# Optimization experiments

Measured on AMD Instinct MI355X. Metric: run time of the kernel, lower is better.

Reference implementation:

```python
import jax, jax.numpy as jnp
import numpy as np

B, T, C, U = 64, 250, 1024, 512


def setup_inputs() -> dict:
    key = jax.random.key(0)
    ks = jax.random.split(key, 9)
    inputs = jax.random.normal(ks[0], (B, T, C), dtype=jnp.float32)
    # contiguous padding mask: True for valid positions
    seq_len = jax.random.randint(ks[1], (B,), T // 2, T + 1)
    mask = jnp.arange(T)[None, :] < seq_len[:, None]
    s_in = 1.0 / np.sqrt(C)
    s_rec = 1.0 / np.sqrt(U)
    Wf = jax.random.normal(ks[2], (C, 3 * U), dtype=jnp.float32) * s_in
    Uf = jax.random.normal(ks[3], (U, 3 * U), dtype=jnp.float32) * s_rec
    bf = jnp.zeros((2, 3 * U), dtype=jnp.float32)  # [input_bias, recurrent_bias] (reset_after=True)
    Wb = jax.random.normal(ks[4], (C, 3 * U), dtype=jnp.float32) * s_in
    Ub = jax.random.normal(ks[5], (U, 3 * U), dtype=jnp.float32) * s_rec
    bb = jnp.zeros((2, 3 * U), dtype=jnp.float32)
    return {"inputs": inputs, "mask": mask, "Wf": Wf, "Uf": Uf, "bf": bf,
            "Wb": Wb, "Ub": Ub, "bb": bb}


def _gru(x_tbc, m_tb, W, Uk, b):
    """Keras GRU v2 (reset_after=True) with masking. x_tbc: [T,B,C], m_tb: [T,B]."""
    # precompute input projections for all timesteps: [T,B,3U]
    xg = jnp.einsum('tbc,cg->tbg', x_tbc, W) + b[0]

    def step(h, inp):
        xg_t, m_t = inp
        hg = h @ Uk + b[1]  # [B,3U]
        xz, xr, xh = jnp.split(xg_t, 3, axis=-1)
        hz, hr, hh = jnp.split(hg, 3, axis=-1)
        z = jax.nn.sigmoid(xz + hz)
        r = jax.nn.sigmoid(xr + hr)
        c = jnp.tanh(xh + r * hh)
        h_new = z * h + (1.0 - z) * c
        h_new = jnp.where(m_t[:, None], h_new, h)  # carry state through masked steps
        return h_new, h_new

    h0 = jnp.zeros((x_tbc.shape[1], Uk.shape[0]), x_tbc.dtype)
    hT, ys = jax.lax.scan(step, h0, (xg, m_tb))
    return ys, hT  # ys: [T,B,U], hT: [B,U]


def reference(inputs, mask, Wf, Uf, bf, Wb, Ub, bb):
    x_t = jnp.transpose(inputs, (1, 0, 2))  # [T,B,C]
    m_t = mask.T  # [T,B]
    y_f, h_f = _gru(x_t, m_t, Wf, Uf, bf)
    # go_backwards: process reversed sequence, then reverse outputs back
    y_b, h_b = _gru(x_t[::-1], m_t[::-1], Wb, Ub, bb)
    y_b = y_b[::-1]
    seq_out = jnp.transpose(jnp.concatenate([y_f, y_b], axis=-1), (1, 0, 2))  # [B,T,2U]
    state_out = jnp.concatenate([h_f, h_b], axis=-1)  # [B,2U]
    return seq_out, state_out
```

## Files before the change

### kernel.cpp

```cpp
#include <hip/hip_runtime.h>
#include <cmath>

#define BB 64
#define TT 250
#define CC 1024
#define GG 1536

typedef unsigned long long u64t;
typedef unsigned int uint32;
typedef unsigned short ushort16;
typedef __attribute__((ext_vector_type(8))) short short8v;
typedef __attribute__((ext_vector_type(4))) float f32x4;

#define O_XGF 0
#define O_XGB 24576000
#define O_UT  49152000
#define O_MF  50724864
#define O_VH  50740864
#define O_WT  51003008
#define O_HINT 54148736

__device__ __forceinline__ unsigned short f2bf(float f) {
  unsigned u = __float_as_uint(f);
  return (unsigned short)((u + 0x7fffu + ((u >> 16) & 1u)) >> 16);
}
__device__ __forceinline__ float bf2f(unsigned short h) {
  return __uint_as_float((unsigned)h << 16);
}
__device__ __forceinline__ void cvt2(float a, float b, uint32& hi, uint32& lo) {
  unsigned short ha = f2bf(a), hb = f2bf(b);
  hi = (uint32)ha | ((uint32)hb << 16);
  lo = (uint32)f2bf(a - bf2f(ha)) | ((uint32)f2bf(b - bf2f(hb)) << 16);
}

__global__ __launch_bounds__(256) void wt_build(
    const float* __restrict__ Wf, const float* __restrict__ Wb,
    ushort16* __restrict__ wt_hi, ushort16* __restrict__ wt_lo)
{
  __shared__ float tile[64][65];
  const int k0 = blockIdx.x * 64;
  const int n0 = blockIdx.y * 64;
  const int d  = blockIdx.z;
  const float* W = d ? Wb : Wf;
  const int l = threadIdx.x & 63, w = threadIdx.x >> 6;
  #pragma unroll
  for (int j = 0; j < 16; j++) {
    int r = j*4 + w;
    tile[r][l] = W[(size_t)(k0+r)*GG + n0 + l];
  }
  __syncthreads();
  #pragma unroll
  for (int j = 0; j < 16; j++) {
    int r = j*4 + w;
    float f = tile[l][r];
    unsigned short h = f2bf(f);
    size_t o = (size_t)(d*GG + n0 + r)*1024 + k0 + l;
    wt_hi[o] = h;
    wt_lo[o] = f2bf(f - bf2f(h));
  }
}

#define LDFRAG(dst, arr, row, kg) do { \
    union { uint4 u; short8v s; } r_; \
    r_.u = *(const uint4*)&arr[(row)*40 + ((kg) << 3)]; \
    dst = r_.s; } while (0)

__global__ __launch_bounds__(256) void fused_prologue(
    const float* __restrict__ X,
    const ushort16* __restrict__ wt_hi, const ushort16* __restrict__ wt_lo,
    const float* __restrict__ bf, const float* __restrict__ bb,
    float* __restrict__ xgf, float* __restrict__ xgb,
    const unsigned char* __restrict__ mraw,
    float* __restrict__ mf, u64t* __restrict__ vh, uint32* __restrict__ hints,
    const float* __restrict__ Uf, const float* __restrict__ Ub,
    float* __restrict__ ut)
{
  __shared__ __align__(16) char sm[40960];
  const int tid = threadIdx.x;
  const int bidx = blockIdx.x;

  if (bidx >= 3512) {
    float (*tile)[65] = (float(*)[65])sm;
    const int q  = bidx - 3512;
    const int k0 = (q & 7) * 64;
    const int n0 = ((q >> 3) % 24) * 64;
    const int d  = q / 192;
    const float* Um = d ? Ub : Uf;
    const int l = tid & 63, w = tid >> 6;
    #pragma unroll
    for (int j = 0; j < 16; j++) {
      int r = j*4 + w;
      tile[r][l] = Um[(size_t)(k0+r)*GG + n0 + l];
    }
    __syncthreads();
    #pragma unroll
    for (int j = 0; j < 16; j++) {
      int r = j*4 + w;
      int n = n0 + r, u = n & 511, g = n >> 9;
      ut[(size_t)(((d << 9) | u)*3 + g)*512 + k0 + l] = tile[l][r];
    }
    return;
  }
  if (bidx >= 3000) {
    int idx = (bidx - 3000) * 256 + tid;
    if (idx < 131072)
      __hip_atomic_store(&vh[idx], 0ULL, __ATOMIC_RELAXED, __HIP_MEMORY_SCOPE_AGENT);
    if (idx < 1024)
      __hip_atomic_store(&hints[idx], 0u, __ATOMIC_RELAXED, __HIP_MEMORY_SCOPE_AGENT);
    if (idx < BB*TT) {
      int b = idx / TT, t = idx - b*TT;
      bool bytefmt = (mraw[1] == 1);
      bool mv = bytefmt ? (mraw[idx] != 0) : (((const int*)mraw)[idx] != 0);
      mf[t*BB + b] = mv ? 1.0f : 0.0f;
    }
    return;
  }

  ushort16* Ah = (ushort16*)sm;
  ushort16* Al = Ah + 128*40;
  ushort16* Bh = Al + 128*40;
  ushort16* Bl = Bh + 128*40;
  const int l  = tid & 63;
  const int wv = tid >> 6;
  const int wm = wv & 1;
  const int wn = wv >> 1;
  const int t0 = (bidx / 24) * 2;
  const int n0 = (bidx % 24) * 128;
  const int d  = (n0 >= GG) ? 1 : 0;
  const int nl0 = n0 - d*GG;
  const float* bias = d ? bb : bf;
  float* xg = d ? xgb : xgf;

  const int sr = tid >> 1;
  const int sk = (tid & 1) << 4;
  const ushort16* whp = wt_hi + (size_t)(d*GG + nl0 + sr)*1024 + sk;
  const ushort16* wlp = wt_lo + (size_t)(d*GG + nl0 + sr)*1024 + sk;
  const int mrow = (sr & 63)*TT + t0 + (sr >> 6);
  const float* xp = X + (size_t)mrow*CC + sk;

  f32x4 acc[4][4];
  #pragma unroll
  for (int i = 0; i < 4; i++)
    #pragma unroll
    for (int j = 0; j < 4; j++) acc[i][j] = (f32x4){0.f,0.f,0.f,0.f};

  const int kg = l >> 4;
  for (int k0 = 0; k0 < CC; k0 += 32) {
    uint4 ha = *(const uint4*)(whp + k0);
    uint4 hb = *(const uint4*)(whp + k0 + 8);
    uint4 la = *(const uint4*)(wlp + k0);
    uint4 lb = *(const uint4*)(wlp + k0 + 8);
    float4 x0 = *(const float4*)(xp + k0);
    float4 x1 = *(const float4*)(xp + k0 + 4);
    float4 x2 = *(const float4*)(xp + k0 + 8);
    float4 x3 = *(const float4*)(xp + k0 + 12);
    __syncthreads();
    {
      *(uint4*)&Ah[sr*40 + sk]     = ha;
      *(uint4*)&Ah[sr*40 + sk + 8] = hb;
      *(uint4*)&Al[sr*40 + sk]     = la;
      *(uint4*)&Al[sr*40 + sk + 8] = lb;
      uint32 bhv[8], blv[8];
      cvt2(x0.x, x0.y, bhv[0], blv[0]); cvt2(x0.z, x0.w, bhv[1], blv[1]);
      cvt2(x1.x, x1.y, bhv[2], blv[2]); cvt2(x1.z, x1.w, bhv[3], blv[3]);
      cvt2(x2.x, x2.y, bhv[4], blv[4]); cvt2(x2.z, x2.w, bhv[5], blv[5]);
      cvt2(x3.x, x3.y, bhv[6], blv[6]); cvt2(x3.z, x3.w, bhv[7], blv[7]);
      *(uint4*)&Bh[sr*40 + sk]     = make_uint4(bhv[0], bhv[1], bhv[2], bhv[3]);
      *(uint4*)&Bh[sr*40 + sk + 8] = make_uint4(bhv[4], bhv[5], bhv[6], bhv[7]);
      *(uint4*)&Bl[sr*40 + sk]     = make_uint4(blv[0], blv[1], blv[2], blv[3]);
      *(uint4*)&Bl[sr*40 + sk + 8] = make_uint4(blv[4], blv[5], blv[6], blv[7]);
    }
    __syncthreads();
    short8v afh[4], afl[4], bfh[4], bfl[4];
    #pragma unroll
    for (int i = 0; i < 4; i++) {
      const int rA = wn*64 + i*16 + (l & 15);
      LDFRAG(afh[i], Ah, rA, kg);
      LDFRAG(afl[i], Al, rA, kg);
      const int rB = wm*64 + i*16 + (l & 15);
      LDFRAG(bfh[i], Bh, rB, kg);
      LDFRAG(bfl[i], Bl, rB, kg);
    }
    #pragma unroll
    for (int i = 0; i < 4; i++)
      #pragma unroll
      for (int j = 0; j < 4; j++) {
        acc[i][j] = __builtin_amdgcn_mfma_f32_16x16x32_bf16(afh[i], bfh[j], acc[i][j], 0, 0, 0);
        acc[i][j] = __builtin_amdgcn_mfma_f32_16x16x32_bf16(afh[i], bfl[j], acc[i][j], 0, 0, 0);
        acc[i][j] = __builtin_amdgcn_mfma_f32_16x16x32_bf16(afl[i], bfh[j], acc[i][j], 0, 0, 0);
      }
  }
  const int t = t0 + wm;
  #pragma unroll
  for (int i = 0; i < 4; i++) {
    const int ugl = wn*64 + i*16 + ((l >> 4) << 2);
    #pragma unroll
    for (int r = 0; r < 4; r++) {
      const int n = nl0 + ugl + r;
      const float bv = bias[n];
      float* orow = xg + (size_t)t*98304 + ((size_t)(n >> 9) << 15) + ((n & 511) << 6);
      #pragma unroll
      for (int j = 0; j < 4; j++)
        orow[j*16 + (l & 15)] = acc[i][j][r] + bv;
    }
  }
}

__global__ __launch_bounds__(512, 2) void gru_scan(
    float* xgf, float* xgb,
    const float* __restrict__ ut, const float* __restrict__ bf,
    const float* __restrict__ bb, const float* __restrict__ mf,
    u64t* vh, uint32* hints, float* __restrict__ out)
{
  __shared__ __align__(16) unsigned short Bhi[2][8192];
  __shared__ __align__(16) unsigned short Blo[2][8192];
  const int tid = threadIdx.x;
  const int l   = tid & 63;
  const int wv  = tid >> 6;
  const int bid = blockIdx.x;
  const int d     = bid >> 6;
  const int mb    = (bid >> 2) & 15;
  const int btile = bid & 3;

  short8v af_hi[16], af_lo[16];
  {
    const int row = (wv << 4) | (l & 15);
    const int g   = row & 3;
    const int ua  = (mb << 5) | (row >> 2);
    const int kg_ = (l >> 4) << 3;
    if (g < 3) {
      const float* ap = ut + (((size_t)(((d << 9) | ua) * 3 + g)) << 9);
      #pragma unroll
      for (int ks = 0; ks < 16; ks++)
        #pragma unroll
        for (int j = 0; j < 8; j++) {
          float f = ap[(ks << 5) + kg_ + j];
          unsigned short h = f2bf(f);
          af_hi[ks][j] = (short)h;
          af_lo[ks][j] = (short)f2bf(f - bf2f(h));
        }
    } else {
      #pragma unroll
      for (int ks = 0; ks < 16; ks++)
        #pragma unroll
        for (int j = 0; j < 8; j++) { af_hi[ks][j] = 0; af_lo[ks][j] = 0; }
    }
  }

  const int u  = (mb << 5) | (wv << 2) | (l >> 4);
  const int b  = (btile << 4) | (l & 15);
  const float* bias = (d ? bb : bf) + GG;
  const float b1z = bias[u], b1r = bias[512+u], b1h = bias[1024+u];
  float* xg = d ? xgb : xgf;
  float hprev = 0.0f;

  const int kc  = tid >> 4;
  const int blw = tid & 15;
  const int cb  = (btile << 4) | blw;
  const int ksub_w = kc >> 1;
  const int qbase  = (kc & 1) << 1;
  const int boff = ((l & 15) << 6) + (((l >> 4) ^ ((l >> 1) & 3)) << 4);

  const u64t* hg = (const u64t*)(hints + (((d << 2) | btile) << 7));
  uint32* myhint = hints + ((((d << 2) | btile) << 7) | (mb << 3) | wv);

  float xzA, xrA, xhA, mA, xzB, xrB, xhB, mB;
  {
    const int tA = d ? (TT-1) : 0;
    const float* p = xg + (size_t)tA*98304 + (u << 6) + b;
    xzA = p[0]; xrA = p[32768]; xhA = p[65536]; mA = mf[tA*BB + b];
    const int tB = d ? (TT-2) : 1;
    const float* q = xg + (size_t)tB*98304 + (u << 6) + b;
    xzB = q[0]; xrB = q[32768]; xhB = q[65536]; mB = mf[tB*BB + b];
  }

  for (int s = 0; s < TT; s++) {
    const unsigned us_ = (unsigned)s;
    const int t = d ? (TT-1-s) : s;
    u64t* vin = vh + (size_t)((((unsigned)s & 1u) << 1) | (unsigned)d) * 32768;

    u64t v[16];
    #pragma unroll
    for (int i = 0; i < 16; i++)
      v[i] = __hip_atomic_load(vin + ((kc << 4) + i)*64 + cb, __ATOMIC_RELAXED, __HIP_MEMORY_SCOPE_AGENT);
    int bad = 0;
    #pragma unroll
    for (int i = 0; i < 16; i++) bad |= ((unsigned)(v[i] >> 32) < us_) ? 1 : 0;
    if (__any(bad)) {
      while (true) {
        u64t hv = __hip_atomic_load(&hg[l], __ATOMIC_RELAXED, __HIP_MEMORY_SCOPE_AGENT);
        if (__all(((unsigned)hv >= us_) && ((unsigned)(hv >> 32) >= us_))) break;
        __builtin_amdgcn_s_sleep(1);
      }
      asm volatile("" ::: "memory");
      while (true) {
        #pragma unroll
        for (int i = 0; i < 16; i++)
          if ((unsigned)(v[i] >> 32) < us_)
            v[i] = __hip_atomic_load(vin + ((kc << 4) + i)*64 + cb, __ATOMIC_RELAXED, __HIP_MEMORY_SCOPE_AGENT);
        int bad2 = 0;
        #pragma unroll
        for (int i = 0; i < 16; i++) bad2 |= ((unsigned)(v[i] >> 32) < us_) ? 1 : 0;
        if (!__any(bad2)) break;
        __builtin_amdgcn_s_sleep(1);
      }
    }

    unsigned short* BhiS = Bhi[s & 1];
    unsigned short* BloS = Blo[s & 1];
    #pragma unroll
    for (int half = 0; half < 2; half++) {
      uint32 hw[4], lw[4];
      #pragma unroll
      for (int p = 0; p < 4; p++) {
        u64t v0 = v[(half << 3) + (p << 1)];
        u64t v1 = v[(half << 3) + (p << 1) + 1];
        hw[p] = (uint32)((v0 >> 16) & 0xffffu) | ((uint32)((v1 >> 16) & 0xffffu) << 16);
        lw[p] = (uint32)(v0 & 0xffffu)         | ((uint32)(v1 & 0xffffu) << 16);
      }
      const int phys = (qbase + half) ^ ((blw >> 1) & 3);
      const int off = (ksub_w << 10) + (blw << 6) + (phys << 4);
      *(uint4*)((char*)BhiS + off) = make_uint4(hw[0], hw[1], hw[2], hw[3]);
      *(uint4*)((char*)BloS + off) = make_uint4(lw[0], lw[1], lw[2], lw[3]);
    }
    __syncthreads();

    float xzC = 0.f, xrC = 0.f, xhC = 0.f, mC = 0.f;
    if (s+2 < TT) {
      const int t2 = d ? (TT-3-s) : (s+2);
      const float* xp = xg + (size_t)t2*98304 + (u << 6) + b;
      xzC = xp[0]; xrC = xp[32768]; xhC = xp[65536];
      mC  = mf[t2*BB + b];
    }

    f32x4 acc0 = {0.f,0.f,0.f,0.f};
    f32x4 acc1 = {0.f,0.f,0.f,0.f};
    f32x4 acc2 = {0.f,0.f,0.f,0.f};
    #pragma unroll
    for (int ks = 0; ks < 16; ks++) {
      short8v bh  = *(const short8v*)((const char*)BhiS + (ks << 10) + boff);
      short8v bl8 = *(const short8v*)((const char*)BloS + (ks << 10) + boff);
      acc0 = __builtin_amdgcn_mfma_f32_16x16x32_bf16(af_hi[ks], bh,  acc0, 0, 0, 0);
      acc1 = __builtin_amdgcn_mfma_f32_16x16x32_bf16(af_hi[ks], bl8, acc1, 0, 0, 0);
      acc2 = __builtin_amdgcn_mfma_f32_16x16x32_bf16(af_lo[ks], bh,  acc2, 0, 0, 0);
    }
    float az = acc0[0] + acc1[0] + acc2[0];
    float ar = acc0[1] + acc1[1] + acc2[1];
    float ah = acc0[2] + acc1[2] + acc2[2];

    float z  = 1.0f / (1.0f + expf(-(xzA + az + b1z)));
    float r  = 1.0f / (1.0f + expf(-(xrA + ar + b1r)));
    float cc = tanhf(xhA + r * (ah + b1h));
    float hn = z*hprev + (1.0f - z)*cc;
    hn = (mA != 0.0f) ? hn : hprev;
    hprev = hn;

    u64t* vout = vh + (size_t)(((((unsigned)s + 1u) & 1u) << 1) | (unsigned)d) * 32768;
    unsigned short hh = f2bf(hn);
    unsigned short hl = f2bf(hn - bf2f(hh));
    u64t pk = ((u64t)(unsigned)(s+1) << 32) | ((u64t)hh << 16) | (u64t)hl;
    __hip_atomic_store(&vout[(u << 6) | b], pk, __ATOMIC_RELAXED, __HIP_MEMORY_SCOPE_AGENT);
    asm volatile("" ::: "memory");
    if (l == 0)
      __hip_atomic_store(myhint, (uint32)(s + 1), __ATOMIC_RELAXED, __HIP_MEMORY_SCOPE_AGENT);
    xg[(size_t)t*98304 + ((size_t)u << 6) + b] = hn;
    xzA = xzB; xrA = xrB; xhA = xhB; mA = mB;
    xzB = xzC; xrB = xrC; xhB = xhC; mB = mC;
  }
  out[16384000ull + ((size_t)b << 10) + (d << 9) + u] = hprev;
}

__global__ __launch_bounds__(256) void y_transpose(
    const float* __restrict__ xgf, const float* __restrict__ xgb,
    float* __restrict__ out)
{
  __shared__ float tile[64][65];
  const int t  = blockIdx.x;
  const int ch = blockIdx.y;
  const int d  = ch >> 3, uc = ch & 7;
  const float* src = (d ? xgb : xgf) + (size_t)t*98304 + (size_t)uc*4096;
  const int lane = threadIdx.x & 63, w = threadIdx.x >> 6;
  #pragma unroll
  for (int j = 0; j < 16; j++) {
    int r = j*4 + w;
    tile[r][lane] = src[r*64 + lane];
  }
  __syncthreads();
  #pragma unroll
  for (int j = 0; j < 16; j++) {
    int b = j*4 + w;
    out[((size_t)b*TT + t)*1024 + (d << 9) + (uc << 6) + lane] = tile[lane][b];
  }
}

extern "C" void kernel_launch(void* const* d_in, const int* in_sizes, int n_in,
                              void* d_out, int out_size, void* d_ws, size_t ws_size,
                              hipStream_t stream) {
  const float* X  = (const float*)d_in[0];
  const unsigned char* Mk = (const unsigned char*)d_in[1];
  const float* Wf = (const float*)d_in[2];
  const float* Uf = (const float*)d_in[3];
  const float* bf = (const float*)d_in[4];
  const float* Wb = (const float*)d_in[5];
  const float* Ub = (const float*)d_in[6];
  const float* bb = (const float*)d_in[7];
  float* out = (float*)d_out;
  float* ws  = (float*)d_ws;
  float* xgf = ws + O_XGF;
  float* xgb = ws + O_XGB;
  float* ut  = ws + O_UT;
  float* mf  = ws + O_MF;
  u64t*  vh  = (u64t*)(ws + O_VH);
  uint32* hints = (uint32*)(ws + O_HINT);
  ushort16* wt_hi = (ushort16*)(ws + O_WT);
  ushort16* wt_lo = wt_hi + (size_t)2*GG*1024;

  wt_build<<<dim3(16, 24, 2), dim3(256), 0, stream>>>(Wf, Wb, wt_hi, wt_lo);
  fused_prologue<<<dim3(3896), dim3(256), 0, stream>>>(
      X, wt_hi, wt_lo, bf, bb, xgf, xgb, Mk, mf, vh, hints, Uf, Ub, ut);
  gru_scan<<<dim3(128), dim3(512), 0, stream>>>(xgf, xgb, ut, bf, bb, mf, vh, hints, out);
  y_transpose<<<dim3(TT, 16), dim3(256), 0, stream>>>(xgf, xgb, out);
}
```

Before: 1.277 ms.

## Pack GRU hidden-state exchange into 32-bit words with 2-bit step tags

The cross-block hidden-state exchange used 64-bit words that held a full step counter plus bf16 hi/lo halves. It now stores 32-bit words: the bf16 high half, plus a low half whose bottom two bits are replaced by a 2-bit step tag. The buffer is re-laid out per (direction, batch tile) group so each thread reads 8 contiguous 64-bit loads instead of 16 strided ones. This halves the global traffic on the latency-critical recurrent sync path. The cost is that the low-order correction loses two mantissa bits, and readiness now depends on a modulo-4 tag rather than a monotonic counter.

```diff
diff --git a/kernel.cpp b/kernel.cpp
--- a/kernel.cpp
+++ b/kernel.cpp
@@ -71,7 +71,7 @@
     const float* __restrict__ bf, const float* __restrict__ bb,
     float* __restrict__ xgf, float* __restrict__ xgb,
     const unsigned char* __restrict__ mraw,
-    float* __restrict__ mf, u64t* __restrict__ vh, uint32* __restrict__ hints,
+    float* __restrict__ mf, uint32* __restrict__ vh2, uint32* __restrict__ hints,
     const float* __restrict__ Uf, const float* __restrict__ Ub,
     float* __restrict__ ut)
 {
@@ -104,7 +104,7 @@
   if (bidx >= 3000) {
     int idx = (bidx - 3000) * 256 + tid;
     if (idx < 131072)
-      __hip_atomic_store(&vh[idx], 0ULL, __ATOMIC_RELAXED, __HIP_MEMORY_SCOPE_AGENT);
+      __hip_atomic_store(&vh2[idx], 0u, __ATOMIC_RELAXED, __HIP_MEMORY_SCOPE_AGENT);
     if (idx < 1024)
       __hip_atomic_store(&hints[idx], 0u, __ATOMIC_RELAXED, __HIP_MEMORY_SCOPE_AGENT);
     if (idx < BB*TT) {
@@ -210,7 +210,7 @@
     float* xgf, float* xgb,
     const float* __restrict__ ut, const float* __restrict__ bf,
     const float* __restrict__ bb, const float* __restrict__ mf,
-    u64t* vh, uint32* hints, float* __restrict__ out)
+    uint32* vh2, uint32* hints, float* __restrict__ out)
 {
   __shared__ __align__(16) unsigned short Bhi[2][8192];
   __shared__ __align__(16) unsigned short Blo[2][8192];
@@ -221,6 +221,7 @@
   const int d     = bid >> 6;
   const int mb    = (bid >> 2) & 15;
   const int btile = bid & 3;
+  const int grp   = (d << 2) | btile;
 
   short8v af_hi[16], af_lo[16];
   {
@@ -256,13 +257,13 @@
 
   const int kc  = tid >> 4;
   const int blw = tid & 15;
-  const int cb  = (btile << 4) | blw;
   const int ksub_w = kc >> 1;
   const int qbase  = (kc & 1) << 1;
   const int boff = ((l & 15) << 6) + (((l >> 4) ^ ((l >> 1) & 3)) << 4);
-
-  const u64t* hg = (const u64t*)(hints + (((d << 2) | btile) << 7));
-  uint32* myhint = hints + ((((d << 2) | btile) << 7) | (mb << 3) | wv);
+  const int ldbase = blw*256 + kc*8;
+
+  const u64t* hg = (const u64t*)(hints + (grp << 7));
+  uint32* myhint = hints + ((grp << 7) | (mb << 3) | wv);
 
   float xzA, xrA, xhA, mA, xzB, xrB, xhB, mB;
   {
@@ -275,18 +276,20 @@
   }
 
   for (int s = 0; s < TT; s++) {
-    const unsigned us_ = (unsigned)s;
+    const unsigned tg = (unsigned)s & 3u;
     const int t = d ? (TT-1-s) : s;
-    u64t* vin = vh + (size_t)((((unsigned)s & 1u) << 1) | (unsigned)d) * 32768;
-
-    u64t v[16];
-    #pragma unroll
-    for (int i = 0; i < 16; i++)
-      v[i] = __hip_atomic_load(vin + ((kc << 4) + i)*64 + cb, __ATOMIC_RELAXED, __HIP_MEMORY_SCOPE_AGENT);
+    u64t* vin = (u64t*)(vh2 + ((size_t)((((unsigned)s & 1u) << 3) | (unsigned)grp) << 13));
+
+    u64t v[8];
+    #pragma unroll
+    for (int i = 0; i < 8; i++)
+      v[i] = __hip_atomic_load(vin + ldbase + i, __ATOMIC_RELAXED, __HIP_MEMORY_SCOPE_AGENT);
     int bad = 0;
     #pragma unroll
-    for (int i = 0; i < 16; i++) bad |= ((unsigned)(v[i] >> 32) < us_) ? 1 : 0;
+    for (int i = 0; i < 8; i++)
+      bad |= (((unsigned)v[i] & 3u) != tg) | (((unsigned)(v[i] >> 32) & 3u) != tg);
     if (__any(bad)) {
+      const unsigned us_ = (unsigned)s;
       while (true) {
         u64t hv = __hip_atomic_load(&hg[l], __ATOMIC_RELAXED, __HIP_MEMORY_SCOPE_AGENT);
         if (__all(((unsigned)hv >= us_) && ((unsigned)(hv >> 32) >= us_))) break;
@@ -295,12 +298,13 @@
       asm volatile("" ::: "memory");
       while (true) {
         #pragma unroll
-        for (int i = 0; i < 16; i++)
-          if ((unsigned)(v[i] >> 32) < us_)
-            v[i] = __hip_atomic_load(vin + ((kc << 4) + i)*64 + cb, __ATOMIC_RELAXED, __HIP_MEMORY_SCOPE_AGENT);
+        for (int i = 0; i < 8; i++)
+          if ((((unsigned)v[i] & 3u) != tg) | (((unsigned)(v[i] >> 32) & 3u) != tg))
+            v[i] = __hip_atomic_load(vin + ldbase + i, __ATOMIC_RELAXED, __HIP_MEMORY_SCOPE_AGENT);
         int bad2 = 0;
         #pragma unroll
-        for (int i = 0; i < 16; i++) bad2 |= ((unsigned)(v[i] >> 32) < us_) ? 1 : 0;
+        for (int i = 0; i < 8; i++)
+          bad2 |= (((unsigned)v[i] & 3u) != tg) | (((unsigned)(v[i] >> 32) & 3u) != tg);
         if (!__any(bad2)) break;
         __builtin_amdgcn_s_sleep(1);
       }
@@ -313,10 +317,11 @@
       uint32 hw[4], lw[4];
       #pragma unroll
       for (int p = 0; p < 4; p++) {
-        u64t v0 = v[(half << 3) + (p << 1)];
-        u64t v1 = v[(half << 3) + (p << 1) + 1];
-        hw[p] = (uint32)((v0 >> 16) & 0xffffu) | ((uint32)((v1 >> 16) & 0xffffu) << 16);
-        lw[p] = (uint32)(v0 & 0xffffu)         | ((uint32)(v1 & 0xffffu) << 16);
+        u64t vv = v[(half << 2) + p];
+        uint32 w0 = (uint32)vv;
+        uint32 w1 = (uint32)(vv >> 32);
+        hw[p] = (w0 >> 16) | (w1 & 0xffff0000u);
+        lw[p] = (w0 & 0xfffcu) | ((w1 & 0xfffcu) << 16);
       }
       const int phys = (qbase + half) ^ ((blw >> 1) & 3);
       const int off = (ksub_w << 10) + (blw << 6) + (phys << 4);
@@ -355,11 +360,11 @@
     hn = (mA != 0.0f) ? hn : hprev;
     hprev = hn;
 
-    u64t* vout = vh + (size_t)(((((unsigned)s + 1u) & 1u) << 1) | (unsigned)d) * 32768;
+    uint32* vout = vh2 + ((size_t)(((((unsigned)s + 1u) & 1u) << 3) | (unsigned)grp) << 13);
     unsigned short hh = f2bf(hn);
     unsigned short hl = f2bf(hn - bf2f(hh));
-    u64t pk = ((u64t)(unsigned)(s+1) << 32) | ((u64t)hh << 16) | (u64t)hl;
-    __hip_atomic_store(&vout[(u << 6) | b], pk, __ATOMIC_RELAXED, __HIP_MEMORY_SCOPE_AGENT);
+    uint32 pk = ((uint32)hh << 16) | ((uint32)hl & 0xfffcu) | (((uint32)(s+1)) & 3u);
+    __hip_atomic_store(&vout[((l & 15) << 9) | u], pk, __ATOMIC_RELAXED, __HIP_MEMORY_SCOPE_AGENT);
     asm volatile("" ::: "memory");
     if (l == 0)
       __hip_atomic_store(myhint, (uint32)(s + 1), __ATOMIC_RELAXED, __HIP_MEMORY_SCOPE_AGENT);
@@ -410,14 +415,14 @@
   float* xgb = ws + O_XGB;
   float* ut  = ws + O_UT;
   float* mf  = ws + O_MF;
-  u64t*  vh  = (u64t*)(ws + O_VH);
+  uint32* vh2 = (uint32*)(ws + O_VH);
   uint32* hints = (uint32*)(ws + O_HINT);
   ushort16* wt_hi = (ushort16*)(ws + O_WT);
   ushort16* wt_lo = wt_hi + (size_t)2*GG*1024;
 
   wt_build<<<dim3(16, 24, 2), dim3(256), 0, stream>>>(Wf, Wb, wt_hi, wt_lo);
   fused_prologue<<<dim3(3896), dim3(256), 0, stream>>>(
-      X, wt_hi, wt_lo, bf, bb, xgf, xgb, Mk, mf, vh, hints, Uf, Ub, ut);
-  gru_scan<<<dim3(128), dim3(512), 0, stream>>>(xgf, xgb, ut, bf, bb, mf, vh, hints, out);
+      X, wt_hi, wt_lo, bf, bb, xgf, xgb, Mk, mf, vh2, hints, Uf, Ub, ut);
+  gru_scan<<<dim3(128), dim3(512), 0, stream>>>(xgf, xgb, ut, bf, bb, mf, vh2, hints, out);
   y_transpose<<<dim3(TT, 16), dim3(256), 0, stream>>>(xgf, xgb, out);
 }
```

Result: slower. 1.723 ms (+34.9%).
